# Kernel optimization log

Hardware: AMD Instinct MI355X
Metric: run time of the kernel (lower is better)

The kernel has to match this reference:

```python
import jax, jax.numpy as jnp
import numpy as np

B, N, F = 2, 512, 128
NUM_BASIS = 4


def _mlp(x, W1, b1, W2, b2, W3, b3):
    # two hidden ReLU layers, linear output -> [..., NUM_BASIS]
    h = jax.nn.relu(x @ W1 + b1)
    h = jax.nn.relu(h @ W2 + b2)
    return h @ W3 + b3


def setup_inputs() -> dict:
    key = jax.random.key(0)
    ks = jax.random.split(key, 12)
    s = 0.05  # keep activations O(1)
    inp = {
        "pointwise_features": jax.random.normal(ks[0], (B, N, F), jnp.float32),
        "relative_features": jax.random.normal(ks[1], (B, N, N, F), jnp.float32),
        "pointwise_basis": jax.random.normal(ks[2], (B, N, NUM_BASIS, 3), jnp.float32),
        "relative_basis": jax.random.normal(ks[3], (B, N, N, NUM_BASIS, 3), jnp.float32),
        "pw_W1": jax.random.normal(ks[4], (F, 128), jnp.float32) * s,
        "pw_b1": jnp.zeros((128,), jnp.float32),
        "pw_W2": jax.random.normal(ks[5], (128, 128), jnp.float32) * s,
        "pw_b2": jnp.zeros((128,), jnp.float32),
        "pw_W3": jax.random.normal(ks[6], (128, NUM_BASIS), jnp.float32) * s,
        "pw_b3": jnp.zeros((NUM_BASIS,), jnp.float32),
        "rel_W1": jax.random.normal(ks[7], (F, 128), jnp.float32) * s,
        "rel_b1": jnp.zeros((128,), jnp.float32),
        "rel_W2": jax.random.normal(ks[8], (128, 128), jnp.float32) * s,
        "rel_b2": jnp.zeros((128,), jnp.float32),
        "rel_W3": jax.random.normal(ks[9], (128, NUM_BASIS), jnp.float32) * s,
        "rel_b3": jnp.zeros((NUM_BASIS,), jnp.float32),
        # last 64 atoms are padding (masked) in every batch element
        "masked_elements": jnp.broadcast_to(jnp.arange(N) >= N - 64, (B, N)),
    }
    return inp


def reference(pointwise_features, relative_features, pointwise_basis, relative_basis,
              pw_W1, pw_b1, pw_W2, pw_b2, pw_W3, pw_b3,
              rel_W1, rel_b1, rel_W2, rel_b2, rel_W3, rel_b3,
              masked_elements):
    unmasked = ~masked_elements                      # [B, N]
    num_atoms = unmasked.sum(-1).astype(pointwise_features.dtype)  # [B]

    # pointwise_shift: [B, N, K, 3]
    pw_scale = _mlp(pointwise_features, pw_W1, pw_b1, pw_W2, pw_b2, pw_W3, pw_b3)
    pointwise_shift = pointwise_basis * pw_scale[..., None]

    # relative_shift: [B, N, N, K, 3], mask over j, mean over j
    rel_scale = _mlp(relative_features, rel_W1, rel_b1, rel_W2, rel_b2, rel_W3, rel_b3)
    relative_shift = relative_basis * rel_scale[..., None]
    relative_shift = relative_shift * unmasked[:, None, :, None, None]
    relative_shift = relative_shift.sum(-3) / num_atoms[:, None, None, None]  # [B, N, K, 3]

    all_shifts = pointwise_shift + relative_shift
    shift = all_shifts.sum(-2) / num_atoms[:, None, None]  # [B, N, 3]
    return shift
```

## Files before the change

kernel.cpp:

```cpp
#include <hip/hip_runtime.h>
#include <stdint.h>

#define LDK 136

typedef __attribute__((ext_vector_type(4))) float f32x4;
typedef __attribute__((ext_vector_type(8))) short bf16x8;

__device__ inline unsigned short f2bf_rtne(float f) {
    union { float f; unsigned u; } v; v.f = f;
    unsigned u = v.u;
    u += 0x7fffu + ((u >> 16) & 1u);
    return (unsigned short)(u >> 16);
}

__global__ void prep_kernel(const float* __restrict__ relW1, const float* __restrict__ relW2,
                            const float* __restrict__ pwW1, const float* __restrict__ pwW2,
                            const float* __restrict__ relW3, const float* __restrict__ pwW3,
                            const void* __restrict__ maskp,
                            float* __restrict__ maskf, float* __restrict__ na,
                            int* __restrict__ gflag, float* __restrict__ out,
                            unsigned short* __restrict__ w1T_rel, unsigned short* __restrict__ w2T_rel,
                            unsigned short* __restrict__ w1T_pw, unsigned short* __restrict__ w2T_pw,
                            unsigned short* __restrict__ w3T_rel, unsigned short* __restrict__ w3T_pw) {
    int t = threadIdx.x;
    const float* srcs[4] = {relW1, relW2, pwW1, pwW2};
    unsigned short* dsts[4] = {w1T_rel, w2T_rel, w1T_pw, w2T_pw};
    int e0 = blockIdx.x * 1024 + t;
#pragma unroll
    for (int i = 0; i < 4; ++i) {
        int e = e0 + i * 256;
        int mat = e >> 14, o = e & 16383;
        int n = o >> 7, k = o & 127;
        dsts[mat][o] = f2bf_rtne(srcs[mat][k * 128 + n]);
    }
    if (blockIdx.x == 1) {
        for (int i = t; i < 2048; i += 256) {
            int r = i >> 7, h = i & 127;
            w3T_rel[i] = (r < 4) ? f2bf_rtne(relW3[h * 4 + r]) : (unsigned short)0;
            w3T_pw[i]  = (r < 4) ? f2bf_rtne(pwW3[h * 4 + r])  : (unsigned short)0;
        }
    }
    if (blockIdx.x == 2) {
        for (int i = t; i < 3072; i += 256) out[i] = 0.f;
    }
    if (blockIdx.x == 0) {
        __shared__ int anyb;
        __shared__ float cnt[2];
        if (t == 0) anyb = 0;
        if (t < 2) cnt[t] = 0.f;
        __syncthreads();
        const unsigned char* mb = (const unsigned char*)maskp;
        int la = 0;
        for (int i = t; i < 1024; i += 256) la |= mb[i];
        if (la) atomicOr(&anyb, 1);
        __syncthreads();
        bool isbyte = (anyb != 0);
        const int* mi = (const int*)maskp;
        float loc0 = 0.f, loc1 = 0.f;
        for (int i = t; i < 1024; i += 256) {
            int v = isbyte ? (int)mb[i] : mi[i];
            float um = (v != 0) ? 0.f : 1.f;
            maskf[i] = um;
            if (i < 512) loc0 += um; else loc1 += um;
        }
        atomicAdd(&cnt[0], loc0);
        atomicAdd(&cnt[1], loc1);
        __syncthreads();
        if (t < 2) na[t] = cnt[t];
        if (t < 16) {
            float s = 0.f;
            for (int j = 0; j < 64; ++j) s += maskf[t * 64 + j];
            gflag[t] = (s > 0.f) ? 1 : 0;
        }
    }
}

__global__ __launch_bounds__(256, 2)
void mlp_kernel(const float* __restrict__ Xrel, const float* __restrict__ Xpw,
                const unsigned short* __restrict__ w1Tr, const unsigned short* __restrict__ w2Tr,
                const unsigned short* __restrict__ w3Tr,
                const unsigned short* __restrict__ w1Tp, const unsigned short* __restrict__ w2Tp,
                const unsigned short* __restrict__ w3Tp,
                const float* __restrict__ b1r, const float* __restrict__ b2r, const float* __restrict__ b3r,
                const float* __restrict__ b1p, const float* __restrict__ b2p, const float* __restrict__ b3p,
                const float* __restrict__ rel_basis, const float* __restrict__ pw_basis,
                const float* __restrict__ maskf, const float* __restrict__ na,
                const int* __restrict__ gflag,
                float* __restrict__ out) {
    __shared__ short xs[64 * LDK];
    __shared__ short hs[64 * LDK];
    __shared__ float bs1[128], bs2[128], b3s[4];
    __shared__ float Sl[256];
    __shared__ float red[4][4][3];

    int t = threadIdx.x;
    int w = t >> 6, lane = t & 63, q = lane >> 4, col = lane & 15;

    bool isrel = (blockIdx.x >= 4);
    int rb = isrel ? ((int)blockIdx.x - 4) : (int)blockIdx.x;

    const float* X = isrel ? Xrel : Xpw;
    const unsigned short* w1T = isrel ? w1Tr : w1Tp;
    const unsigned short* w2T = isrel ? w2Tr : w2Tp;
    const unsigned short* w3T = isrel ? w3Tr : w3Tp;
    const float* b1 = isrel ? b1r : b1p;
    const float* b2 = isrel ? b2r : b2p;
    const float* b3 = isrel ? b3r : b3p;

    if (t < 128) { bs1[t] = b1[t]; bs2[t] = b2[t]; }
    if (t < 4) b3s[t] = b3[t];

    int b = isrel ? (rb >> 10) : (rb >> 1);
    float NA = na[b];
    float scale = isrel ? (1.f / (NA * NA)) : (1.f / NA);

    int apack = 0x3210, nact = 4;
    if (isrel) {
        apack = 0; nact = 0;
        int gbase = b * 8 + (rb & 1) * 4;
#pragma unroll
        for (int tt = 0; tt < 4; ++tt)
            if (gflag[gbase + tt]) { apack |= tt << (4 * nact); ++nact; }
        if (nact == 0) return;
    }

    bf16x8 w1f[2][4], w2f[2][4], w3f[4];
#pragma unroll
    for (int tn = 0; tn < 2; ++tn)
#pragma unroll
        for (int kc = 0; kc < 4; ++kc) {
            int n = w * 32 + tn * 16 + col;
            int kk = kc * 32 + q * 8;
            w1f[tn][kc] = *(const bf16x8*)&w1T[n * 128 + kk];
            w2f[tn][kc] = *(const bf16x8*)&w2T[n * 128 + kk];
        }
#pragma unroll
    for (int kc = 0; kc < 4; ++kc)
        w3f[kc] = *(const bf16x8*)&w3T[col * 128 + kc * 32 + q * 8];

    long rowbase = (long)rb * 256;
    int r0 = t >> 5, cg = t & 31;
    int arow = t >> 2, ak = t & 3;

    float4 px[8];
    {
        const float4* Xg = (const float4*)(X + (rowbase + (long)(apack & 15) * 64) * 128);
#pragma unroll
        for (int i = 0; i < 8; ++i) px[i] = Xg[(r0 + 8 * i) * 32 + cg];
#pragma unroll
        for (int i = 0; i < 8; ++i) {
            float4 v = px[i];
            short4 s4 = make_short4((short)f2bf_rtne(v.x), (short)f2bf_rtne(v.y),
                                    (short)f2bf_rtne(v.z), (short)f2bf_rtne(v.w));
            *(short4*)&xs[(r0 + 8 * i) * LDK + cg * 4] = s4;
        }
    }
    __syncthreads();

    float p0 = 0.f, p1 = 0.f, p2 = 0.f;

    for (int a = 0; a < nact; ++a) {
        int tile = (apack >> (4 * a)) & 15;
        long trow = rowbase + (long)tile * 64;

        if (a + 1 < nact) {
            int tnx = (apack >> (4 * (a + 1))) & 15;
            const float4* Xg2 = (const float4*)(X + (rowbase + (long)tnx * 64) * 128);
#pragma unroll
            for (int i = 0; i < 8; ++i) px[i] = Xg2[(r0 + 8 * i) * 32 + cg];
        }

        float bas0 = 0.f, bas1 = 0.f, bas2 = 0.f, mrow = 0.f;
        if (isrel) {
            const float* bp = &rel_basis[(trow + arow) * 12 + ak * 3];
            bas0 = bp[0]; bas1 = bp[1]; bas2 = bp[2];
            mrow = maskf[b * 512 + (rb & 1) * 256 + tile * 64 + w * 16 + col];
        }

        f32x4 acc[2][4];
#pragma unroll
        for (int tn = 0; tn < 2; ++tn)
#pragma unroll
            for (int tm = 0; tm < 4; ++tm) acc[tn][tm] = (f32x4)(0.f);
#pragma unroll
        for (int kc = 0; kc < 4; ++kc) {
            bf16x8 bf[4];
#pragma unroll
            for (int tm = 0; tm < 4; ++tm)
                bf[tm] = *(const bf16x8*)&xs[(tm * 16 + col) * LDK + kc * 32 + q * 8];
#pragma unroll
            for (int tn = 0; tn < 2; ++tn)
#pragma unroll
                for (int tm = 0; tm < 4; ++tm)
                    acc[tn][tm] = __builtin_amdgcn_mfma_f32_16x16x32_bf16(w1f[tn][kc], bf[tm], acc[tn][tm], 0, 0, 0);
        }

#pragma unroll
        for (int tn = 0; tn < 2; ++tn)
#pragma unroll
            for (int tm = 0; tm < 4; ++tm) {
                int n0 = w * 32 + tn * 16 + q * 4;
                int m = tm * 16 + col;
                float4 bb = *(const float4*)&bs1[n0];
                short4 s4 = make_short4(
                    (short)f2bf_rtne(fmaxf(acc[tn][tm][0] + bb.x, 0.f)),
                    (short)f2bf_rtne(fmaxf(acc[tn][tm][1] + bb.y, 0.f)),
                    (short)f2bf_rtne(fmaxf(acc[tn][tm][2] + bb.z, 0.f)),
                    (short)f2bf_rtne(fmaxf(acc[tn][tm][3] + bb.w, 0.f)));
                *(short4*)&hs[m * LDK + n0] = s4;
            }
        __syncthreads();

        if (a + 1 < nact) {
#pragma unroll
            for (int i = 0; i < 8; ++i) {
                float4 v = px[i];
                short4 s4 = make_short4((short)f2bf_rtne(v.x), (short)f2bf_rtne(v.y),
                                        (short)f2bf_rtne(v.z), (short)f2bf_rtne(v.w));
                *(short4*)&xs[(r0 + 8 * i) * LDK + cg * 4] = s4;
            }
        }

        f32x4 acc2[2][4];
#pragma unroll
        for (int tn = 0; tn < 2; ++tn)
#pragma unroll
            for (int tm = 0; tm < 4; ++tm) acc2[tn][tm] = (f32x4)(0.f);
#pragma unroll
        for (int kc = 0; kc < 4; ++kc) {
            bf16x8 bf[4];
#pragma unroll
            for (int tm = 0; tm < 4; ++tm)
                bf[tm] = *(const bf16x8*)&hs[(tm * 16 + col) * LDK + kc * 32 + q * 8];
#pragma unroll
            for (int tn = 0; tn < 2; ++tn)
#pragma unroll
                for (int tm = 0; tm < 4; ++tm)
                    acc2[tn][tm] = __builtin_amdgcn_mfma_f32_16x16x32_bf16(w2f[tn][kc], bf[tm], acc2[tn][tm], 0, 0, 0);
        }
        __syncthreads();

#pragma unroll
        for (int tn = 0; tn < 2; ++tn)
#pragma unroll
            for (int tm = 0; tm < 4; ++tm) {
                int n0 = w * 32 + tn * 16 + q * 4;
                int m = tm * 16 + col;
                float4 bb = *(const float4*)&bs2[n0];
                short4 s4 = make_short4(
                    (short)f2bf_rtne(fmaxf(acc2[tn][tm][0] + bb.x, 0.f)),
                    (short)f2bf_rtne(fmaxf(acc2[tn][tm][1] + bb.y, 0.f)),
                    (short)f2bf_rtne(fmaxf(acc2[tn][tm][2] + bb.z, 0.f)),
                    (short)f2bf_rtne(fmaxf(acc2[tn][tm][3] + bb.w, 0.f)));
                *(short4*)&hs[m * LDK + n0] = s4;
            }
        __syncthreads();

        {
            f32x4 a3 = (f32x4)(0.f);
#pragma unroll
            for (int kc = 0; kc < 4; ++kc) {
                bf16x8 hb = *(const bf16x8*)&hs[(w * 16 + col) * LDK + kc * 32 + q * 8];
                a3 = __builtin_amdgcn_mfma_f32_16x16x32_bf16(w3f[kc], hb, a3, 0, 0, 0);
            }
            if (isrel) {
                if (q == 0) {
                    float4 sm = make_float4((a3[0] + b3s[0]) * mrow, (a3[1] + b3s[1]) * mrow,
                                            (a3[2] + b3s[2]) * mrow, (a3[3] + b3s[3]) * mrow);
                    *(float4*)&Sl[(w * 16 + col) * 4] = sm;
                }
            } else if (q == 0) {
                long bi = trow + w * 16 + col;
                float s0 = a3[0] + b3s[0], s1 = a3[1] + b3s[1];
                float s2 = a3[2] + b3s[2], s3 = a3[3] + b3s[3];
                const float* pbp = &pw_basis[bi * 12];
                float o0 = s0 * pbp[0] + s1 * pbp[3] + s2 * pbp[6] + s3 * pbp[9];
                float o1 = s0 * pbp[1] + s1 * pbp[4] + s2 * pbp[7] + s3 * pbp[10];
                float o2 = s0 * pbp[2] + s1 * pbp[5] + s2 * pbp[8] + s3 * pbp[11];
                atomicAdd(&out[bi * 3 + 0], o0 * scale);
                atomicAdd(&out[bi * 3 + 1], o1 * scale);
                atomicAdd(&out[bi * 3 + 2], o2 * scale);
            }
        }
        __syncthreads();

        if (isrel) {
            float sk = Sl[arow * 4 + ak];
            p0 += sk * bas0; p1 += sk * bas1; p2 += sk * bas2;
        }
    }

    if (isrel) {
#pragma unroll
        for (int s = 32; s >= 4; s >>= 1) {
            p0 += __shfl_down(p0, s);
            p1 += __shfl_down(p1, s);
            p2 += __shfl_down(p2, s);
        }
        if (lane < 4) { red[w][lane][0] = p0; red[w][lane][1] = p1; red[w][lane][2] = p2; }
        __syncthreads();
        if (t < 3) {
            float v = 0.f;
#pragma unroll
            for (int ww = 0; ww < 4; ++ww)
#pragma unroll
                for (int k = 0; k < 4; ++k) v += red[ww][k][t];
            atomicAdd(&out[(long)(rb >> 1) * 3 + t], v * scale);
        }
    }
}

extern "C" void kernel_launch(void* const* d_in, const int* in_sizes, int n_in,
                              void* d_out, int out_size, void* d_ws, size_t ws_size,
                              hipStream_t stream) {
    const float* pw_feat   = (const float*)d_in[0];
    const float* rel_feat  = (const float*)d_in[1];
    const float* pw_basis  = (const float*)d_in[2];
    const float* rel_basis = (const float*)d_in[3];
    const float* pw_W1 = (const float*)d_in[4];
    const float* pw_b1 = (const float*)d_in[5];
    const float* pw_W2 = (const float*)d_in[6];
    const float* pw_b2 = (const float*)d_in[7];
    const float* pw_W3 = (const float*)d_in[8];
    const float* pw_b3 = (const float*)d_in[9];
    const float* rel_W1 = (const float*)d_in[10];
    const float* rel_b1 = (const float*)d_in[11];
    const float* rel_W2 = (const float*)d_in[12];
    const float* rel_b2 = (const float*)d_in[13];
    const float* rel_W3 = (const float*)d_in[14];
    const float* rel_b3 = (const float*)d_in[15];
    const void*  maskp  = d_in[16];
    float* out = (float*)d_out;

    char* ws = (char*)d_ws;
    float* maskf = (float*)(ws + 0);
    float* na    = (float*)(ws + 4096);
    int*   gflag = (int*)(ws + 4160);
    unsigned short* w1T_rel = (unsigned short*)(ws + 4352);
    unsigned short* w2T_rel = (unsigned short*)(ws + 37120);
    unsigned short* w1T_pw  = (unsigned short*)(ws + 69888);
    unsigned short* w2T_pw  = (unsigned short*)(ws + 102656);
    unsigned short* w3T_rel = (unsigned short*)(ws + 135424);
    unsigned short* w3T_pw  = (unsigned short*)(ws + 139520);

    prep_kernel<<<64, 256, 0, stream>>>(rel_W1, rel_W2, pw_W1, pw_W2, rel_W3, pw_W3, maskp,
                                        maskf, na, gflag, out,
                                        w1T_rel, w2T_rel, w1T_pw, w2T_pw,
                                        w3T_rel, w3T_pw);
    mlp_kernel<<<2052, 256, 0, stream>>>(rel_feat, pw_feat,
                                         w1T_rel, w2T_rel, w3T_rel,
                                         w1T_pw, w2T_pw, w3T_pw,
                                         rel_b1, rel_b2, rel_b3,
                                         pw_b1, pw_b2, pw_b3,
                                         rel_basis, pw_basis, maskf, na, gflag, out);
}
```

Baseline: 421.7 us.

## Process one 64-row tile per block instead of looping over four tiles

The MLP kernel now gives each block a single 64-row tile, using four times as many blocks, rather than looping over up to four tiles with software prefetch of the next tile. Layer-2 output is written into the freed input buffer, and the basis contraction is done in registers on the q==0 lanes, which removes the Sl staging buffer and one barrier per tile. Launch bounds rise to three blocks per SM to raise occupancy. In exchange, weight fragments are reloaded per tile, cross-tile prefetch is lost, and output atomics increase fourfold for relative rows.

```diff
diff --git a/kernel.cpp b/kernel.cpp
--- a/kernel.cpp
+++ b/kernel.cpp
@@ -75,7 +75,7 @@
     }
 }
 
-__global__ __launch_bounds__(256, 2)
+__global__ __launch_bounds__(256, 3)
 void mlp_kernel(const float* __restrict__ Xrel, const float* __restrict__ Xpw,
                 const unsigned short* __restrict__ w1Tr, const unsigned short* __restrict__ w2Tr,
                 const unsigned short* __restrict__ w3Tr,
@@ -90,14 +90,16 @@
     __shared__ short xs[64 * LDK];
     __shared__ short hs[64 * LDK];
     __shared__ float bs1[128], bs2[128], b3s[4];
-    __shared__ float Sl[256];
-    __shared__ float red[4][4][3];
+    __shared__ float red[4][3];
 
     int t = threadIdx.x;
     int w = t >> 6, lane = t & 63, q = lane >> 4, col = lane & 15;
 
-    bool isrel = (blockIdx.x >= 4);
-    int rb = isrel ? ((int)blockIdx.x - 4) : (int)blockIdx.x;
+    bool isrel = (blockIdx.x >= 16);
+    int tt = isrel ? ((int)blockIdx.x - 16) : (int)blockIdx.x;
+    int b = isrel ? (tt >> 12) : (tt >> 3);
+
+    if (isrel && gflag[(tt >> 12) * 8 + (tt & 7)] == 0) return;
 
     const float* X = isrel ? Xrel : Xpw;
     const unsigned short* w1T = isrel ? w1Tr : w1Tp;
@@ -107,21 +109,14 @@
     const float* b2 = isrel ? b2r : b2p;
     const float* b3 = isrel ? b3r : b3p;
 
-    if (t < 128) { bs1[t] = b1[t]; bs2[t] = b2[t]; }
-    if (t < 4) b3s[t] = b3[t];
-
-    int b = isrel ? (rb >> 10) : (rb >> 1);
-    float NA = na[b];
-    float scale = isrel ? (1.f / (NA * NA)) : (1.f / NA);
-
-    int apack = 0x3210, nact = 4;
-    if (isrel) {
-        apack = 0; nact = 0;
-        int gbase = b * 8 + (rb & 1) * 4;
-#pragma unroll
-        for (int tt = 0; tt < 4; ++tt)
-            if (gflag[gbase + tt]) { apack |= tt << (4 * nact); ++nact; }
-        if (nact == 0) return;
+    long rowbase = (long)tt * 64;
+    int r0 = t >> 5, cg = t & 31;
+
+    float4 px[8];
+    {
+        const float4* Xg = (const float4*)(X + rowbase * 128);
+#pragma unroll
+        for (int i = 0; i < 8; ++i) px[i] = Xg[(r0 + 8 * i) * 32 + cg];
     }
 
     bf16x8 w1f[2][4], w2f[2][4], w3f[4];
@@ -138,174 +133,137 @@
     for (int kc = 0; kc < 4; ++kc)
         w3f[kc] = *(const bf16x8*)&w3T[col * 128 + kc * 32 + q * 8];
 
-    long rowbase = (long)rb * 256;
-    int r0 = t >> 5, cg = t & 31;
-    int arow = t >> 2, ak = t & 3;
-
-    float4 px[8];
+    if (t < 128) { bs1[t] = b1[t]; bs2[t] = b2[t]; }
+    if (t < 4) b3s[t] = b3[t];
+
+    float NA = na[b];
+    float scale = isrel ? (1.f / (NA * NA)) : (1.f / NA);
+
+    int myrow = w * 16 + col;
+    float4 bq0, bq1, bq2; float mrow = 1.f;
+    if (q == 0) {
+        const float* bp = isrel ? &rel_basis[(rowbase + myrow) * 12]
+                                : &pw_basis[(rowbase + myrow) * 12];
+        bq0 = *(const float4*)&bp[0];
+        bq1 = *(const float4*)&bp[4];
+        bq2 = *(const float4*)&bp[8];
+        if (isrel) mrow = maskf[b * 512 + (tt & 7) * 64 + myrow];
+    }
+
+#pragma unroll
+    for (int i = 0; i < 8; ++i) {
+        float4 v = px[i];
+        short4 s4 = make_short4((short)f2bf_rtne(v.x), (short)f2bf_rtne(v.y),
+                                (short)f2bf_rtne(v.z), (short)f2bf_rtne(v.w));
+        *(short4*)&xs[(r0 + 8 * i) * LDK + cg * 4] = s4;
+    }
+    __syncthreads();
+
+    f32x4 acc[2][4];
+#pragma unroll
+    for (int tn = 0; tn < 2; ++tn)
+#pragma unroll
+        for (int tm = 0; tm < 4; ++tm) acc[tn][tm] = (f32x4)(0.f);
+#pragma unroll
+    for (int kc = 0; kc < 4; ++kc) {
+        bf16x8 bf[4];
+#pragma unroll
+        for (int tm = 0; tm < 4; ++tm)
+            bf[tm] = *(const bf16x8*)&xs[(tm * 16 + col) * LDK + kc * 32 + q * 8];
+#pragma unroll
+        for (int tn = 0; tn < 2; ++tn)
+#pragma unroll
+            for (int tm = 0; tm < 4; ++tm)
+                acc[tn][tm] = __builtin_amdgcn_mfma_f32_16x16x32_bf16(w1f[tn][kc], bf[tm], acc[tn][tm], 0, 0, 0);
+    }
+
+#pragma unroll
+    for (int tn = 0; tn < 2; ++tn)
+#pragma unroll
+        for (int tm = 0; tm < 4; ++tm) {
+            int n0 = w * 32 + tn * 16 + q * 4;
+            int m = tm * 16 + col;
+            float4 bb = *(const float4*)&bs1[n0];
+            short4 s4 = make_short4(
+                (short)f2bf_rtne(fmaxf(acc[tn][tm][0] + bb.x, 0.f)),
+                (short)f2bf_rtne(fmaxf(acc[tn][tm][1] + bb.y, 0.f)),
+                (short)f2bf_rtne(fmaxf(acc[tn][tm][2] + bb.z, 0.f)),
+                (short)f2bf_rtne(fmaxf(acc[tn][tm][3] + bb.w, 0.f)));
+            *(short4*)&hs[m * LDK + n0] = s4;
+        }
+    __syncthreads();
+
+    f32x4 acc2[2][4];
+#pragma unroll
+    for (int tn = 0; tn < 2; ++tn)
+#pragma unroll
+        for (int tm = 0; tm < 4; ++tm) acc2[tn][tm] = (f32x4)(0.f);
+#pragma unroll
+    for (int kc = 0; kc < 4; ++kc) {
+        bf16x8 bf[4];
+#pragma unroll
+        for (int tm = 0; tm < 4; ++tm)
+            bf[tm] = *(const bf16x8*)&hs[(tm * 16 + col) * LDK + kc * 32 + q * 8];
+#pragma unroll
+        for (int tn = 0; tn < 2; ++tn)
+#pragma unroll
+            for (int tm = 0; tm < 4; ++tm)
+                acc2[tn][tm] = __builtin_amdgcn_mfma_f32_16x16x32_bf16(w2f[tn][kc], bf[tm], acc2[tn][tm], 0, 0, 0);
+    }
+
+#pragma unroll
+    for (int tn = 0; tn < 2; ++tn)
+#pragma unroll
+        for (int tm = 0; tm < 4; ++tm) {
+            int n0 = w * 32 + tn * 16 + q * 4;
+            int m = tm * 16 + col;
+            float4 bb = *(const float4*)&bs2[n0];
+            short4 s4 = make_short4(
+                (short)f2bf_rtne(fmaxf(acc2[tn][tm][0] + bb.x, 0.f)),
+                (short)f2bf_rtne(fmaxf(acc2[tn][tm][1] + bb.y, 0.f)),
+                (short)f2bf_rtne(fmaxf(acc2[tn][tm][2] + bb.z, 0.f)),
+                (short)f2bf_rtne(fmaxf(acc2[tn][tm][3] + bb.w, 0.f)));
+            *(short4*)&xs[m * LDK + n0] = s4;
+        }
+    __syncthreads();
+
+    float p0 = 0.f, p1 = 0.f, p2 = 0.f;
     {
-        const float4* Xg = (const float4*)(X + (rowbase + (long)(apack & 15) * 64) * 128);
-#pragma unroll
-        for (int i = 0; i < 8; ++i) px[i] = Xg[(r0 + 8 * i) * 32 + cg];
-#pragma unroll
-        for (int i = 0; i < 8; ++i) {
-            float4 v = px[i];
-            short4 s4 = make_short4((short)f2bf_rtne(v.x), (short)f2bf_rtne(v.y),
-                                    (short)f2bf_rtne(v.z), (short)f2bf_rtne(v.w));
-            *(short4*)&xs[(r0 + 8 * i) * LDK + cg * 4] = s4;
-        }
-    }
-    __syncthreads();
-
-    float p0 = 0.f, p1 = 0.f, p2 = 0.f;
-
-    for (int a = 0; a < nact; ++a) {
-        int tile = (apack >> (4 * a)) & 15;
-        long trow = rowbase + (long)tile * 64;
-
-        if (a + 1 < nact) {
-            int tnx = (apack >> (4 * (a + 1))) & 15;
-            const float4* Xg2 = (const float4*)(X + (rowbase + (long)tnx * 64) * 128);
-#pragma unroll
-            for (int i = 0; i < 8; ++i) px[i] = Xg2[(r0 + 8 * i) * 32 + cg];
-        }
-
-        float bas0 = 0.f, bas1 = 0.f, bas2 = 0.f, mrow = 0.f;
-        if (isrel) {
-            const float* bp = &rel_basis[(trow + arow) * 12 + ak * 3];
-            bas0 = bp[0]; bas1 = bp[1]; bas2 = bp[2];
-            mrow = maskf[b * 512 + (rb & 1) * 256 + tile * 64 + w * 16 + col];
-        }
-
-        f32x4 acc[2][4];
-#pragma unroll
-        for (int tn = 0; tn < 2; ++tn)
-#pragma unroll
-            for (int tm = 0; tm < 4; ++tm) acc[tn][tm] = (f32x4)(0.f);
+        f32x4 a3 = (f32x4)(0.f);
 #pragma unroll
         for (int kc = 0; kc < 4; ++kc) {
-            bf16x8 bf[4];
-#pragma unroll
-            for (int tm = 0; tm < 4; ++tm)
-                bf[tm] = *(const bf16x8*)&xs[(tm * 16 + col) * LDK + kc * 32 + q * 8];
-#pragma unroll
-            for (int tn = 0; tn < 2; ++tn)
-#pragma unroll
-                for (int tm = 0; tm < 4; ++tm)
-                    acc[tn][tm] = __builtin_amdgcn_mfma_f32_16x16x32_bf16(w1f[tn][kc], bf[tm], acc[tn][tm], 0, 0, 0);
-        }
-
-#pragma unroll
-        for (int tn = 0; tn < 2; ++tn)
-#pragma unroll
-            for (int tm = 0; tm < 4; ++tm) {
-                int n0 = w * 32 + tn * 16 + q * 4;
-                int m = tm * 16 + col;
-                float4 bb = *(const float4*)&bs1[n0];
-                short4 s4 = make_short4(
-                    (short)f2bf_rtne(fmaxf(acc[tn][tm][0] + bb.x, 0.f)),
-                    (short)f2bf_rtne(fmaxf(acc[tn][tm][1] + bb.y, 0.f)),
-                    (short)f2bf_rtne(fmaxf(acc[tn][tm][2] + bb.z, 0.f)),
-                    (short)f2bf_rtne(fmaxf(acc[tn][tm][3] + bb.w, 0.f)));
-                *(short4*)&hs[m * LDK + n0] = s4;
+            bf16x8 hb = *(const bf16x8*)&xs[(w * 16 + col) * LDK + kc * 32 + q * 8];
+            a3 = __builtin_amdgcn_mfma_f32_16x16x32_bf16(w3f[kc], hb, a3, 0, 0, 0);
+        }
+        if (q == 0) {
+            float s0 = (a3[0] + b3s[0]) * mrow;
+            float s1 = (a3[1] + b3s[1]) * mrow;
+            float s2 = (a3[2] + b3s[2]) * mrow;
+            float s3 = (a3[3] + b3s[3]) * mrow;
+            p0 = s0 * bq0.x + s1 * bq0.w + s2 * bq1.z + s3 * bq2.y;
+            p1 = s0 * bq0.y + s1 * bq1.x + s2 * bq1.w + s3 * bq2.z;
+            p2 = s0 * bq0.z + s1 * bq1.y + s2 * bq2.x + s3 * bq2.w;
+            if (!isrel) {
+                long bi = rowbase + myrow;
+                atomicAdd(&out[bi * 3 + 0], p0 * scale);
+                atomicAdd(&out[bi * 3 + 1], p1 * scale);
+                atomicAdd(&out[bi * 3 + 2], p2 * scale);
             }
-        __syncthreads();
-
-        if (a + 1 < nact) {
-#pragma unroll
-            for (int i = 0; i < 8; ++i) {
-                float4 v = px[i];
-                short4 s4 = make_short4((short)f2bf_rtne(v.x), (short)f2bf_rtne(v.y),
-                                        (short)f2bf_rtne(v.z), (short)f2bf_rtne(v.w));
-                *(short4*)&xs[(r0 + 8 * i) * LDK + cg * 4] = s4;
-            }
-        }
-
-        f32x4 acc2[2][4];
-#pragma unroll
-        for (int tn = 0; tn < 2; ++tn)
-#pragma unroll
-            for (int tm = 0; tm < 4; ++tm) acc2[tn][tm] = (f32x4)(0.f);
-#pragma unroll
-        for (int kc = 0; kc < 4; ++kc) {
-            bf16x8 bf[4];
-#pragma unroll
-            for (int tm = 0; tm < 4; ++tm)
-                bf[tm] = *(const bf16x8*)&hs[(tm * 16 + col) * LDK + kc * 32 + q * 8];
-#pragma unroll
-            for (int tn = 0; tn < 2; ++tn)
-#pragma unroll
-                for (int tm = 0; tm < 4; ++tm)
-                    acc2[tn][tm] = __builtin_amdgcn_mfma_f32_16x16x32_bf16(w2f[tn][kc], bf[tm], acc2[tn][tm], 0, 0, 0);
-        }
-        __syncthreads();
-
-#pragma unroll
-        for (int tn = 0; tn < 2; ++tn)
-#pragma unroll
-            for (int tm = 0; tm < 4; ++tm) {
-                int n0 = w * 32 + tn * 16 + q * 4;
-                int m = tm * 16 + col;
-                float4 bb = *(const float4*)&bs2[n0];
-                short4 s4 = make_short4(
-                    (short)f2bf_rtne(fmaxf(acc2[tn][tm][0] + bb.x, 0.f)),
-                    (short)f2bf_rtne(fmaxf(acc2[tn][tm][1] + bb.y, 0.f)),
-                    (short)f2bf_rtne(fmaxf(acc2[tn][tm][2] + bb.z, 0.f)),
-                    (short)f2bf_rtne(fmaxf(acc2[tn][tm][3] + bb.w, 0.f)));
-                *(short4*)&hs[m * LDK + n0] = s4;
-            }
-        __syncthreads();
-
-        {
-            f32x4 a3 = (f32x4)(0.f);
-#pragma unroll
-            for (int kc = 0; kc < 4; ++kc) {
-                bf16x8 hb = *(const bf16x8*)&hs[(w * 16 + col) * LDK + kc * 32 + q * 8];
-                a3 = __builtin_amdgcn_mfma_f32_16x16x32_bf16(w3f[kc], hb, a3, 0, 0, 0);
-            }
-            if (isrel) {
-                if (q == 0) {
-                    float4 sm = make_float4((a3[0] + b3s[0]) * mrow, (a3[1] + b3s[1]) * mrow,
-                                            (a3[2] + b3s[2]) * mrow, (a3[3] + b3s[3]) * mrow);
-                    *(float4*)&Sl[(w * 16 + col) * 4] = sm;
-                }
-            } else if (q == 0) {
-                long bi = trow + w * 16 + col;
-                float s0 = a3[0] + b3s[0], s1 = a3[1] + b3s[1];
-                float s2 = a3[2] + b3s[2], s3 = a3[3] + b3s[3];
-                const float* pbp = &pw_basis[bi * 12];
-                float o0 = s0 * pbp[0] + s1 * pbp[3] + s2 * pbp[6] + s3 * pbp[9];
-                float o1 = s0 * pbp[1] + s1 * pbp[4] + s2 * pbp[7] + s3 * pbp[10];
-                float o2 = s0 * pbp[2] + s1 * pbp[5] + s2 * pbp[8] + s3 * pbp[11];
-                atomicAdd(&out[bi * 3 + 0], o0 * scale);
-                atomicAdd(&out[bi * 3 + 1], o1 * scale);
-                atomicAdd(&out[bi * 3 + 2], o2 * scale);
-            }
-        }
-        __syncthreads();
-
-        if (isrel) {
-            float sk = Sl[arow * 4 + ak];
-            p0 += sk * bas0; p1 += sk * bas1; p2 += sk * bas2;
         }
     }
 
     if (isrel) {
 #pragma unroll
-        for (int s = 32; s >= 4; s >>= 1) {
+        for (int s = 32; s > 0; s >>= 1) {
             p0 += __shfl_down(p0, s);
             p1 += __shfl_down(p1, s);
             p2 += __shfl_down(p2, s);
         }
-        if (lane < 4) { red[w][lane][0] = p0; red[w][lane][1] = p1; red[w][lane][2] = p2; }
+        if (lane == 0) { red[w][0] = p0; red[w][1] = p1; red[w][2] = p2; }
         __syncthreads();
         if (t < 3) {
-            float v = 0.f;
-#pragma unroll
-            for (int ww = 0; ww < 4; ++ww)
-#pragma unroll
-                for (int k = 0; k < 4; ++k) v += red[ww][k][t];
-            atomicAdd(&out[(long)(rb >> 1) * 3 + t], v * scale);
+            float v = red[0][t] + red[1][t] + red[2][t] + red[3][t];
+            atomicAdd(&out[(long)(tt >> 3) * 3 + t], v * scale);
         }
     }
 }
@@ -347,7 +305,7 @@
                                         maskf, na, gflag, out,
                                         w1T_rel, w2T_rel, w1T_pw, w2T_pw,
                                         w3T_rel, w3T_pw);
-    mlp_kernel<<<2052, 256, 0, stream>>>(rel_feat, pw_feat,
+    mlp_kernel<<<8208, 256, 0, stream>>>(rel_feat, pw_feat,
                                          w1T_rel, w2T_rel, w3T_rel,
                                          w1T_pw, w2T_pw, w3T_pw,
                                          rel_b1, rel_b2, rel_b3,
```

After: 429.3 us. No clear change (+1.8%).

## Double-buffer hidden tile and contract basis in registers to drop per-tile barrier

Applied to the files above, without the earlier changes.

The hidden-activation LDS buffer is now double-buffered by tile parity, so the trailing __syncthreads at the end of each tile iteration can be removed. The per-row basis contraction is done directly in registers by the q==0 lanes using vector loads of the 12 basis floats. This replaces the Sl scratch array and the spread-out per-thread basis loads. The goal is fewer barriers and less LDS traffic per tile, at the cost of extra LDS for the second buffer and reduced parallelism in the final contraction.

```diff
diff --git a/kernel.cpp b/kernel.cpp
--- a/kernel.cpp
+++ b/kernel.cpp
@@ -88,10 +88,9 @@
                 const int* __restrict__ gflag,
                 float* __restrict__ out) {
     __shared__ short xs[64 * LDK];
-    __shared__ short hs[64 * LDK];
+    __shared__ short hs[2][64 * LDK];
     __shared__ float bs1[128], bs2[128], b3s[4];
-    __shared__ float Sl[256];
-    __shared__ float red[4][4][3];
+    __shared__ float red[4][3];
 
     int t = threadIdx.x;
     int w = t >> 6, lane = t & 63, q = lane >> 4, col = lane & 15;
@@ -140,7 +139,7 @@
 
     long rowbase = (long)rb * 256;
     int r0 = t >> 5, cg = t & 31;
-    int arow = t >> 2, ak = t & 3;
+    int myrow = w * 16 + col;
 
     float4 px[8];
     {
@@ -162,6 +161,7 @@
     for (int a = 0; a < nact; ++a) {
         int tile = (apack >> (4 * a)) & 15;
         long trow = rowbase + (long)tile * 64;
+        int hp = a & 1;
 
         if (a + 1 < nact) {
             int tnx = (apack >> (4 * (a + 1))) & 15;
@@ -170,11 +170,14 @@
             for (int i = 0; i < 8; ++i) px[i] = Xg2[(r0 + 8 * i) * 32 + cg];
         }
 
-        float bas0 = 0.f, bas1 = 0.f, bas2 = 0.f, mrow = 0.f;
-        if (isrel) {
-            const float* bp = &rel_basis[(trow + arow) * 12 + ak * 3];
-            bas0 = bp[0]; bas1 = bp[1]; bas2 = bp[2];
-            mrow = maskf[b * 512 + (rb & 1) * 256 + tile * 64 + w * 16 + col];
+        float4 bq0, bq1, bq2; float mrow = 1.f;
+        if (q == 0) {
+            const float* bp = isrel ? &rel_basis[(trow + myrow) * 12]
+                                    : &pw_basis[(trow + myrow) * 12];
+            bq0 = *(const float4*)&bp[0];
+            bq1 = *(const float4*)&bp[4];
+            bq2 = *(const float4*)&bp[8];
+            if (isrel) mrow = maskf[b * 512 + (rb & 1) * 256 + tile * 64 + myrow];
         }
 
         f32x4 acc[2][4];
@@ -207,7 +210,7 @@
                     (short)f2bf_rtne(fmaxf(acc[tn][tm][1] + bb.y, 0.f)),
                     (short)f2bf_rtne(fmaxf(acc[tn][tm][2] + bb.z, 0.f)),
                     (short)f2bf_rtne(fmaxf(acc[tn][tm][3] + bb.w, 0.f)));
-                *(short4*)&hs[m * LDK + n0] = s4;
+                *(short4*)&hs[hp][m * LDK + n0] = s4;
             }
         __syncthreads();
 
@@ -231,7 +234,7 @@
             bf16x8 bf[4];
 #pragma unroll
             for (int tm = 0; tm < 4; ++tm)
-                bf[tm] = *(const bf16x8*)&hs[(tm * 16 + col) * LDK + kc * 32 + q * 8];
+                bf[tm] = *(const bf16x8*)&hs[hp][(tm * 16 + col) * LDK + kc * 32 + q * 8];
 #pragma unroll
             for (int tn = 0; tn < 2; ++tn)
 #pragma unroll
@@ -252,7 +255,7 @@
                     (short)f2bf_rtne(fmaxf(acc2[tn][tm][1] + bb.y, 0.f)),
                     (short)f2bf_rtne(fmaxf(acc2[tn][tm][2] + bb.z, 0.f)),
                     (short)f2bf_rtne(fmaxf(acc2[tn][tm][3] + bb.w, 0.f)));
-                *(short4*)&hs[m * LDK + n0] = s4;
+                *(short4*)&hs[hp][m * LDK + n0] = s4;
             }
         __syncthreads();
 
@@ -260,51 +263,40 @@
             f32x4 a3 = (f32x4)(0.f);
 #pragma unroll
             for (int kc = 0; kc < 4; ++kc) {
-                bf16x8 hb = *(const bf16x8*)&hs[(w * 16 + col) * LDK + kc * 32 + q * 8];
+                bf16x8 hb = *(const bf16x8*)&hs[hp][(w * 16 + col) * LDK + kc * 32 + q * 8];
                 a3 = __builtin_amdgcn_mfma_f32_16x16x32_bf16(w3f[kc], hb, a3, 0, 0, 0);
             }
-            if (isrel) {
-                if (q == 0) {
-                    float4 sm = make_float4((a3[0] + b3s[0]) * mrow, (a3[1] + b3s[1]) * mrow,
-                                            (a3[2] + b3s[2]) * mrow, (a3[3] + b3s[3]) * mrow);
-                    *(float4*)&Sl[(w * 16 + col) * 4] = sm;
+            if (q == 0) {
+                float s0 = (a3[0] + b3s[0]) * mrow;
+                float s1 = (a3[1] + b3s[1]) * mrow;
+                float s2 = (a3[2] + b3s[2]) * mrow;
+                float s3 = (a3[3] + b3s[3]) * mrow;
+                float o0 = s0 * bq0.x + s1 * bq0.w + s2 * bq1.z + s3 * bq2.y;
+                float o1 = s0 * bq0.y + s1 * bq1.x + s2 * bq1.w + s3 * bq2.z;
+                float o2 = s0 * bq0.z + s1 * bq1.y + s2 * bq2.x + s3 * bq2.w;
+                if (isrel) {
+                    p0 += o0; p1 += o1; p2 += o2;
+                } else {
+                    long bi = trow + myrow;
+                    atomicAdd(&out[bi * 3 + 0], o0 * scale);
+                    atomicAdd(&out[bi * 3 + 1], o1 * scale);
+                    atomicAdd(&out[bi * 3 + 2], o2 * scale);
                 }
-            } else if (q == 0) {
-                long bi = trow + w * 16 + col;
-                float s0 = a3[0] + b3s[0], s1 = a3[1] + b3s[1];
-                float s2 = a3[2] + b3s[2], s3 = a3[3] + b3s[3];
-                const float* pbp = &pw_basis[bi * 12];
-                float o0 = s0 * pbp[0] + s1 * pbp[3] + s2 * pbp[6] + s3 * pbp[9];
-                float o1 = s0 * pbp[1] + s1 * pbp[4] + s2 * pbp[7] + s3 * pbp[10];
-                float o2 = s0 * pbp[2] + s1 * pbp[5] + s2 * pbp[8] + s3 * pbp[11];
-                atomicAdd(&out[bi * 3 + 0], o0 * scale);
-                atomicAdd(&out[bi * 3 + 1], o1 * scale);
-                atomicAdd(&out[bi * 3 + 2], o2 * scale);
-            }
-        }
-        __syncthreads();
-
-        if (isrel) {
-            float sk = Sl[arow * 4 + ak];
-            p0 += sk * bas0; p1 += sk * bas1; p2 += sk * bas2;
+            }
         }
     }
 
     if (isrel) {
 #pragma unroll
-        for (int s = 32; s >= 4; s >>= 1) {
+        for (int s = 32; s > 0; s >>= 1) {
             p0 += __shfl_down(p0, s);
             p1 += __shfl_down(p1, s);
             p2 += __shfl_down(p2, s);
         }
-        if (lane < 4) { red[w][lane][0] = p0; red[w][lane][1] = p1; red[w][lane][2] = p2; }
+        if (lane == 0) { red[w][0] = p0; red[w][1] = p1; red[w][2] = p2; }
         __syncthreads();
         if (t < 3) {
-            float v = 0.f;
-#pragma unroll
-            for (int ww = 0; ww < 4; ++ww)
-#pragma unroll
-                for (int k = 0; k < 4; ++k) v += red[ww][k][t];
+            float v = red[0][t] + red[1][t] + red[2][t] + red[3][t];
             atomicAdd(&out[(long)(rb >> 1) * 3 + t], v * scale);
         }
     }
```

Result: slower. 432.4 us (+2.5%).
